# Kernel optimization log

Hardware: AMD Instinct MI355X
Metric: run time of the kernel (lower is better)

The kernel has to match this reference:

```python
import jax, jax.numpy as jnp
import numpy as np
import math

B, NQ, NS, K = 4, 4096, 16384, 16
P, IN, D = 3, 128, 256
H = D // 16   # nhead = out_dim // 16 = 16
HD = D // H   # head_dim = 16
RADIUS = 4.0
EPS = 1e-5


def _ln(x, g, b):
    m = jnp.mean(x, -1, keepdims=True)
    v = jnp.mean((x - m) ** 2, -1, keepdims=True)
    return (x - m) / jnp.sqrt(v + EPS) * g + b


def _pos_enc(x, W_pos, b_pos):
    # LearnablePositionalEncoding: cat([x, cos(Linear(2*pi*x))], -1)
    return jnp.concatenate([x, jnp.cos((2.0 * math.pi * x) @ W_pos + b_pos)], axis=-1)


def setup_inputs() -> dict:
    key = jax.random.key(0)
    ks = jax.random.split(key, 24)
    f32 = jnp.float32

    def w(k, shape):
        return jax.random.uniform(k, shape, f32, -1.0, 1.0) / np.float32(np.sqrt(shape[0]))

    inp = {}
    inp['q_pts'] = jax.random.normal(ks[0], (B, NQ, P), f32)
    inp['s_pts'] = jax.random.normal(ks[1], (B, NS, P), f32)
    inp['src_feats'] = jax.random.normal(ks[2], (B, NS, IN), f32)
    inp['query_feats'] = jax.random.normal(ks[3], (B, NQ, IN), f32)
    # shared proj (in_dim != out_dim, skip_dim=None -> skip_proj is the same Linear)
    inp['W_proj'] = w(ks[4], (IN, D)); inp['b_proj'] = jnp.zeros((D,), f32)
    # positional encoding Linear(p_dim, out_dim - p_dim)
    inp['W_pos'] = w(ks[5], (P, D - P)); inp['b_pos'] = jnp.zeros((D - P,), f32)
    # TransformerDecoderLayer (norm_first) params
    inp['ln1_g'] = jnp.ones((D,), f32); inp['ln1_b'] = jnp.zeros((D,), f32)
    inp['sa_Wv'] = w(ks[6], (D, D)); inp['sa_bv'] = jnp.zeros((D,), f32)
    inp['sa_Wo'] = w(ks[7], (D, D)); inp['sa_bo'] = jnp.zeros((D,), f32)
    inp['ln2_g'] = jnp.ones((D,), f32); inp['ln2_b'] = jnp.zeros((D,), f32)
    inp['ca_Wq'] = w(ks[8], (D, D)); inp['ca_bq'] = jnp.zeros((D,), f32)
    inp['ca_Wk'] = w(ks[9], (D, D)); inp['ca_bk'] = jnp.zeros((D,), f32)
    inp['ca_Wv'] = w(ks[10], (D, D)); inp['ca_bv'] = jnp.zeros((D,), f32)
    inp['ca_Wo'] = w(ks[11], (D, D)); inp['ca_bo'] = jnp.zeros((D,), f32)
    inp['ln3_g'] = jnp.ones((D,), f32); inp['ln3_b'] = jnp.zeros((D,), f32)
    inp['W1'] = w(ks[12], (D, D)); inp['b1'] = jnp.zeros((D,), f32)
    inp['W2'] = w(ks[13], (D, D)); inp['b2'] = jnp.zeros((D,), f32)
    inp['neighb_inds'] = jax.random.randint(ks[14], (B, NQ, K), 0, NS)
    return inp


def reference(q_pts, s_pts, src_feats, query_feats, W_proj, b_proj, W_pos, b_pos,
              ln1_g, ln1_b, sa_Wv, sa_bv, sa_Wo, sa_bo, ln2_g, ln2_b,
              ca_Wq, ca_bq, ca_Wk, ca_bk, ca_Wv, ca_bv, ca_Wo, ca_bo,
              ln3_g, ln3_b, W1, b1, W2, b2, neighb_inds):
    # append shadow point at 1e6 with zero feature row
    s_pts_ = jnp.concatenate([s_pts, jnp.full_like(s_pts[:, :1, :], 1e6)], axis=1)   # [B,NS+1,P]
    src_ = jnp.concatenate([src_feats, jnp.zeros_like(src_feats[:, :1, :])], axis=1)  # [B,NS+1,IN]
    src_p = src_ @ W_proj + b_proj            # proj(src_feats)  [B,NS+1,D]
    qf = query_feats @ W_proj + b_proj        # skip_proj == proj (skip_dim=None)
    inds = neighb_inds % (NS + 1)
    flat = inds.reshape(B, -1, 1)             # [B, NQ*K, 1]
    neighbors = jnp.take_along_axis(s_pts_, jnp.broadcast_to(flat, (B, NQ * K, P)), axis=1).reshape(B, NQ, K, P)
    neighb_x = jnp.take_along_axis(src_p, jnp.broadcast_to(flat, (B, NQ * K, D)), axis=1).reshape(B, NQ, K, D)
    neighbors = neighbors - q_pts[:, :, None, :]
    neighb_x = neighb_x + _pos_enc(neighbors / RADIUS, W_pos, b_pos)
    query_x = qf + _pos_enc(jnp.zeros_like(q_pts), W_pos, b_pos)
    mask = jnp.linalg.norm(neighbors, axis=-1) > RADIUS   # [B,NQ,K], True = invalid key

    x = query_x   # [B,NQ,D]: a length-1 target sequence per query point
    # --- self-attention block (seq len 1 -> softmax == 1 -> only V/O projections matter) ---
    h = _ln(x, ln1_g, ln1_b)
    x = x + (h @ sa_Wv + sa_bv) @ sa_Wo + sa_bo
    # --- cross-attention to K gathered neighbors ---
    h = _ln(x, ln2_g, ln2_b)
    q = (h @ ca_Wq + ca_bq).reshape(B, NQ, H, HD)
    kk = (neighb_x @ ca_Wk + ca_bk).reshape(B, NQ, K, H, HD)
    vv = (neighb_x @ ca_Wv + ca_bv).reshape(B, NQ, K, H, HD)
    scores = jnp.einsum('bnhd,bnkhd->bnhk', q, kk) / np.float32(np.sqrt(HD))
    scores = jnp.where(mask[:, :, None, :], jnp.float32(-1e9), scores)
    att = jax.nn.softmax(scores, axis=-1)
    ctx = jnp.einsum('bnhk,bnkhd->bnhd', att, vv).reshape(B, NQ, D)
    x = x + ctx @ ca_Wo + ca_bo
    # --- feed-forward (dim_feedforward == d_model, relu) ---
    h = _ln(x, ln3_g, ln3_b)
    x = x + jax.nn.relu(h @ W1 + b1) @ W2 + b2
    # original zeroes any NaNs (fully-masked rows); shapes chosen so this is a no-op
    return jnp.nan_to_num(x)
```

## Files before the change

### kernel.cpp

```cpp
#include <hip/hip_runtime.h>
#include <hip/hip_bf16.h>
#include <math.h>
#include <stdint.h>

typedef __attribute__((ext_vector_type(8))) short short8;
typedef __attribute__((ext_vector_type(4))) float floatx4;

#define DEVI __device__ __forceinline__

DEVI float b2f(unsigned short u) {
    union { unsigned int i; float f; } v; v.i = ((unsigned int)u) << 16; return v.f;
}
DEVI unsigned short f2b(float f) {
    unsigned int x = __float_as_uint(f);
    unsigned int r = (x + 0x7fffu + ((x >> 16) & 1u)) >> 16;
    return (unsigned short)r;
}

#define GLD16(gp, lp)                                                            \
    __builtin_amdgcn_global_load_lds(                                            \
        (__attribute__((address_space(1))) unsigned int*)(gp),                   \
        (__attribute__((address_space(3))) unsigned int*)(lp), 16, 0, 0)

static constexpr int NQ = 4096, NS = 16384;
static constexpr int NROW_Q = 4 * NQ;
static constexpr int NROW_S = 4 * NS;
static constexpr float INV2PI = 0.15915494309189535f;

__global__ void k_prep(const float* Wproj, const float* saWv, const float* saWo,
                       const float* caWq, const float* caWk, const float* caWv,
                       const float* caWo, const float* W1, const float* W2,
                       const float* b_pos,
                       unsigned short* wTproj, unsigned short* wTsaWv, unsigned short* wTsaWo,
                       unsigned short* wTcaWq, unsigned short* wTkv, unsigned short* wTcaWo,
                       unsigned short* wTW1, unsigned short* wTW2, float* penc0)
{
    int z = blockIdx.z;
    if (z == 9) {
        if (blockIdx.x == 0 && blockIdx.y == 0) {
            int c = threadIdx.y * 16 + threadIdx.x;
            float v = 0.f;
            if (c >= 3) {
                float rev = b_pos[c - 3] * INV2PI;
                rev -= floorf(rev);
                v = __builtin_amdgcn_cosf(rev);
            }
            penc0[c] = v;
        }
        return;
    }
    int n = blockIdx.x * 16 + threadIdx.x;
    int k = blockIdx.y * 16 + threadIdx.y;
    const float* src; unsigned short* dst; int K = 256;
    switch (z) {
        case 0: src = Wproj; dst = wTproj; K = 128; break;
        case 1: src = saWv;  dst = wTsaWv; break;
        case 2: src = saWo;  dst = wTsaWo; break;
        case 3: src = caWq;  dst = wTcaWq; break;
        case 4: src = caWk;  dst = wTkv;   break;
        case 5: src = caWv;  dst = wTkv + 256 * 256; break;
        case 6: src = caWo;  dst = wTcaWo; break;
        case 7: src = W1;    dst = wTW1;   break;
        default: src = W2;   dst = wTW2;   break;
    }
    if (k < K) dst[(size_t)n * K + k] = f2b(src[(size_t)k * 256 + n]);
}

__global__ void k_scale(const float* b_pos, float* bp2)
{
    int i = blockIdx.x * blockDim.x + threadIdx.x;
    if (i < 253) bp2[i] = b_pos[i] * INV2PI;
}

__global__ void k_cvt(const float* in, unsigned short* out, int n4)
{
    int i = blockIdx.x * blockDim.x + threadIdx.x;
    int stride = gridDim.x * blockDim.x;
    for (; i < n4; i += stride) {
        float4 v = ((const float4*)in)[i];
        unsigned long long p =
              (unsigned long long)f2b(v.x)
            | ((unsigned long long)f2b(v.y) << 16)
            | ((unsigned long long)f2b(v.z) << 32)
            | ((unsigned long long)f2b(v.w) << 48);
        ((unsigned long long*)out)[i] = p;
    }
}

template<int EPI>
__global__ __launch_bounds__(256, 2)
void k_gemm(const unsigned short* A, const unsigned short* BT, const float* bias,
            const float* extra, void* outp, int M, int N, int K)
{
    __shared__ alignas(16) unsigned short lA[128 * 64];
    __shared__ alignas(16) unsigned short lB[64 * 64];
    const int tid = threadIdx.x;
    const int wave = tid >> 6, lane = tid & 63;
    const int m0 = blockIdx.x * 128, n0 = blockIdx.y * 64;
    const int wm = (wave >> 1) * 64, wn = (wave & 1) * 32;
    floatx4 acc[4][2] = {};

    for (int kt = 0; kt < K; kt += 64) {
        __syncthreads();
        #pragma unroll
        for (int c = 0; c < 4; ++c) {
            int o = (tid + c * 256) * 16;
            int row = o >> 7, inner = o & 127;
            int srk = inner ^ ((row & 7) << 4);
            GLD16((const char*)A + ((size_t)(m0 + row) * K + kt) * 2 + srk, (char*)lA + o);
        }
        #pragma unroll
        for (int c = 0; c < 2; ++c) {
            int o = (tid + c * 256) * 16;
            int row = o >> 7, inner = o & 127;
            int srk = inner ^ ((row & 7) << 4);
            GLD16((const char*)BT + ((size_t)(n0 + row) * K + kt) * 2 + srk, (char*)lB + o);
        }
        __syncthreads();
        #pragma unroll
        for (int kc = 0; kc < 2; ++kc) {
            const int kb = kc * 64 + ((lane >> 4) << 4);
            short8 bf[2];
            #pragma unroll
            for (int nf = 0; nf < 2; ++nf) {
                int nn = wn + nf * 16 + (lane & 15);
                bf[nf] = *(const short8*)((const char*)lB + nn * 128 + (kb ^ ((nn & 7) << 4)));
            }
            #pragma unroll
            for (int mf = 0; mf < 4; ++mf) {
                int rr = wm + mf * 16 + (lane & 15);
                short8 af = *(const short8*)((const char*)lA + rr * 128 + (kb ^ ((rr & 7) << 4)));
                acc[mf][0] = __builtin_amdgcn_mfma_f32_16x16x32_bf16(af, bf[0], acc[mf][0], 0, 0, 0);
                acc[mf][1] = __builtin_amdgcn_mfma_f32_16x16x32_bf16(af, bf[1], acc[mf][1], 0, 0, 0);
            }
        }
    }
    #pragma unroll
    for (int mf = 0; mf < 4; ++mf)
        #pragma unroll
        for (int nf = 0; nf < 2; ++nf)
            #pragma unroll
            for (int r = 0; r < 4; ++r) {
                int row = m0 + wm + mf * 16 + ((lane >> 4) << 2) + r;
                int col = n0 + wn + nf * 16 + (lane & 15);
                float v = acc[mf][nf][r] + bias[col];
                if (EPI == 4) v += extra[(size_t)row * N + col];
                if (EPI == 1) v = fmaxf(v, 0.f);
                if (EPI == 4) {
                    if (isnan(v)) v = 0.f;
                    else if (isinf(v)) v = v > 0.f ? 3.402823466e38f : -3.402823466e38f;
                }
                if (EPI == 0 || EPI == 1)
                    ((unsigned short*)outp)[(size_t)row * N + col] = f2b(v);
                else
                    ((float*)outp)[(size_t)row * N + col] = v;
            }
}

template<int EPI2>
__global__ __launch_bounds__(256, 2)
void k_gemm_ln(const unsigned short* A, const unsigned short* BT, const float* bias,
               const float* extra, const float* lng, const float* lnb,
               float* outf, unsigned short* outb, int M, int K)
{
    __shared__ alignas(16) unsigned short lA[64 * 64];
    __shared__ alignas(16) unsigned short lB[256 * 64];
    const int tid = threadIdx.x, wave = tid >> 6, lane = tid & 63;
    const int l15 = lane & 15, lg = lane >> 4;
    const int m0 = blockIdx.x * 64;
    floatx4 acc[16] = {};

    for (int kt = 0; kt < K; kt += 64) {
        __syncthreads();
        #pragma unroll
        for (int c = 0; c < 2; ++c) {
            int o = (tid + c * 256) * 16;
            int row = o >> 7, inner = o & 127;
            int srk = inner ^ ((row & 7) << 4);
            GLD16((const char*)A + ((size_t)(m0 + row) * K + kt) * 2 + srk, (char*)lA + o);
        }
        #pragma unroll
        for (int c = 0; c < 8; ++c) {
            int o = (tid + c * 256) * 16;
            int row = o >> 7, inner = o & 127;
            int srk = inner ^ ((row & 7) << 4);
            GLD16((const char*)BT + ((size_t)row * K + kt) * 2 + srk, (char*)lB + o);
        }
        __syncthreads();
        #pragma unroll
        for (int kc = 0; kc < 2; ++kc) {
            const int kb = kc * 64 + (lg << 4);
            int rr = wave * 16 + l15;
            short8 af = *(const short8*)((const char*)lA + rr * 128 + (kb ^ ((rr & 7) << 4)));
            #pragma unroll
            for (int nf = 0; nf < 16; ++nf) {
                int nn = nf * 16 + l15;
                short8 bf = *(const short8*)((const char*)lB + nn * 128 + (kb ^ ((nn & 7) << 4)));
                acc[nf] = __builtin_amdgcn_mfma_f32_16x16x32_bf16(af, bf, acc[nf], 0, 0, 0);
            }
        }
    }

    #pragma unroll
    for (int nf = 0; nf < 16; ++nf) {
        int col = nf * 16 + l15;
        float bi = bias[col] + (EPI2 == 0 ? extra[col] : 0.f);
        #pragma unroll
        for (int r = 0; r < 4; ++r) {
            int row = m0 + wave * 16 + lg * 4 + r;
            float v = acc[nf][r] + bi;
            if (EPI2 == 1) v += extra[(size_t)row * 256 + col];
            acc[nf][r] = v;
            outf[(size_t)row * 256 + col] = v;
        }
    }
    float mean[4], inv[4];
    #pragma unroll
    for (int r = 0; r < 4; ++r) {
        float s = 0.f;
        #pragma unroll
        for (int nf = 0; nf < 16; ++nf) s += acc[nf][r];
        #pragma unroll
        for (int t = 1; t <= 8; t <<= 1) s += __shfl_xor(s, t);
        mean[r] = s * (1.f / 256.f);
        float q = 0.f;
        #pragma unroll
        for (int nf = 0; nf < 16; ++nf) { float d = acc[nf][r] - mean[r]; q += d * d; }
        #pragma unroll
        for (int t = 1; t <= 8; t <<= 1) q += __shfl_xor(q, t);
        inv[r] = 1.0f / sqrtf(q * (1.f / 256.f) + 1e-5f);
    }
    #pragma unroll
    for (int nf = 0; nf < 16; ++nf) {
        int col = nf * 16 + l15;
        float g = lng[col], b = lnb[col];
        #pragma unroll
        for (int r = 0; r < 4; ++r) {
            int row = m0 + wave * 16 + lg * 4 + r;
            outb[(size_t)row * 256 + col] = f2b((acc[nf][r] - mean[r]) * inv[r] * g + b);
        }
    }
}

__global__ __launch_bounds__(256, 3)
void k_attn(const unsigned short* srcp, const unsigned short* qb, const int* inds,
            const float* s_pts, const float* q_pts, const float* W_pos, const float* bp2,
            const unsigned short* wTkv, const float* bv, unsigned short* ctx)
{
    __shared__ alignas(16) unsigned short nx[64 * 256];
    __shared__ alignas(16) float att_lds[4 * 16 * 16];
    __shared__ alignas(16) float dist_lds[64];
    const int tid = threadIdx.x, wave = tid >> 6, lane = tid & 63;
    const int qbase = blockIdx.x * 4;
    const int l15 = lane & 15, lg = lane >> 4;

    float qv[4][4], bvv[4];
    #pragma unroll
    for (int mf = 0; mf < 4; ++mf)
        #pragma unroll
        for (int nf = 0; nf < 4; ++nf)
            qv[mf][nf] = b2f(qb[(size_t)(qbase + mf) * 256 + (wave * 4 + nf) * 16 + l15]) * 0.25f;
    #pragma unroll
    for (int nf = 0; nf < 4; ++nf) bvv[nf] = bv[(wave * 4 + nf) * 16 + l15];

    {
        int r = tid >> 2, sub = tid & 3;
        int qi = qbase + (r >> 4);
        int bb = qi >> 12;
        int k = r & 15;
        int raw = inds[((size_t)qi << 4) + k];
        int idx = raw % (NS + 1); if (idx < 0) idx += NS + 1;
        bool shadow = (idx == NS);
        const int c0 = sub * 64;
        const unsigned short* srow = srcp + ((size_t)bb * NS + (shadow ? 0 : idx)) * 256 + c0;
        short8 sv[8];
        #pragma unroll
        for (int j = 0; j < 8; ++j) sv[j] = *(const short8*)(srow + j * 8);

        float px = q_pts[(size_t)qi * 3], py = q_pts[(size_t)qi * 3 + 1], pz = q_pts[(size_t)qi * 3 + 2];
        float sx, sy, sz;
        if (shadow) { sx = sy = sz = 1e6f; }
        else {
            const float* sp = s_pts + ((size_t)bb * NS + idx) * 3;
            sx = sp[0]; sy = sp[1]; sz = sp[2];
        }
        float tx = (sx - px) * 0.25f, ty = (sy - py) * 0.25f, tz = (sz - pz) * 0.25f;
        if (sub == 0) dist_lds[r] = tx * tx + ty * ty + tz * tz;

        #pragma unroll
        for (int cc = 0; cc < 64; cc += 8) {
            short8 vals;
            #pragma unroll
            for (int j = 0; j < 8; ++j) {
                int c = c0 + cc + j;
                float pe;
                if (c == 0) pe = tx;
                else if (c == 1) pe = ty;
                else if (c == 2) pe = tz;
                else {
                    int jj = c - 3;
                    float rev = fmaf(tx, W_pos[jj],
                                fmaf(ty, W_pos[253 + jj],
                                fmaf(tz, W_pos[506 + jj], bp2[jj])));
                    rev -= floorf(rev);
                    pe = __builtin_amdgcn_cosf(rev);
                }
                float sval = shadow ? 0.f : b2f((unsigned short)sv[cc / 8][j]);
                vals[j] = (short)f2b(sval + pe);
            }
            int byte = (c0 + cc) * 2;
            *(short8*)((char*)nx + r * 512 + (byte ^ ((r & 7) << 4))) = vals;
        }
    }
    __syncthreads();

    const int wn = wave * 64;
    floatx4 acc[4][4];

    #pragma unroll
    for (int mf = 0; mf < 4; ++mf)
        #pragma unroll
        for (int nf = 0; nf < 4; ++nf) acc[mf][nf] = floatx4{0.f, 0.f, 0.f, 0.f};

    #pragma unroll 2
    for (int kt = 0; kt < 8; ++kt) {
        const int kb = kt * 64 + (lg << 4);
        short8 bfr[4];
        #pragma unroll
        for (int nf = 0; nf < 4; ++nf) {
            int nn = wn + nf * 16 + l15;
            bfr[nf] = *(const short8*)((const char*)wTkv + (size_t)nn * 512 + kt * 64 + (lg << 4));
        }
        #pragma unroll
        for (int mf = 0; mf < 4; ++mf) {
            int rr = mf * 16 + l15;
            short8 af = *(const short8*)((const char*)nx + rr * 512 + (kb ^ ((rr & 7) << 4)));
            #pragma unroll
            for (int nf = 0; nf < 4; ++nf)
                acc[mf][nf] = __builtin_amdgcn_mfma_f32_16x16x32_bf16(af, bfr[nf], acc[mf][nf], 0, 0, 0);
        }
    }

    {
        #pragma unroll
        for (int mf = 0; mf < 4; ++mf) {
            float4 d4 = *(const float4*)&dist_lds[mf * 16 + lg * 4];
            float dd4[4] = {d4.x, d4.y, d4.z, d4.w};
            #pragma unroll
            for (int nf = 0; nf < 4; ++nf) {
                float s[4];
                #pragma unroll
                for (int rr = 0; rr < 4; ++rr) s[rr] = acc[mf][nf][rr] * qv[mf][nf];
                #pragma unroll
                for (int t = 1; t <= 8; t <<= 1)
                    #pragma unroll
                    for (int rr = 0; rr < 4; ++rr) s[rr] += __shfl_xor(s[rr], t);
                #pragma unroll
                for (int rr = 0; rr < 4; ++rr)
                    s[rr] = (dd4[rr] > 1.0f) ? -1e9f : s[rr];
                float m = fmaxf(fmaxf(s[0], s[1]), fmaxf(s[2], s[3]));
                m = fmaxf(m, __shfl_xor(m, 16));
                m = fmaxf(m, __shfl_xor(m, 32));
                float p[4], su = 0.f;
                #pragma unroll
                for (int rr = 0; rr < 4; ++rr) { p[rr] = __expf(s[rr] - m); su += p[rr]; }
                su += __shfl_xor(su, 16);
                su += __shfl_xor(su, 32);
                float inv = __builtin_amdgcn_rcpf(su);
                if (l15 == 0) {
                    float4 a4 = {p[0] * inv, p[1] * inv, p[2] * inv, p[3] * inv};
                    *(float4*)&att_lds[(mf * 16 + wave * 4 + nf) * 16 + lg * 4] = a4;
                }
            }
        }
    }

    #pragma unroll
    for (int mf = 0; mf < 4; ++mf)
        #pragma unroll
        for (int nf = 0; nf < 4; ++nf) acc[mf][nf] = floatx4{0.f, 0.f, 0.f, 0.f};

    #pragma unroll 2
    for (int kt = 0; kt < 8; ++kt) {
        const int kb = kt * 64 + (lg << 4);
        short8 bfr[4];
        #pragma unroll
        for (int nf = 0; nf < 4; ++nf) {
            int nn = 256 + wn + nf * 16 + l15;
            bfr[nf] = *(const short8*)((const char*)wTkv + (size_t)nn * 512 + kt * 64 + (lg << 4));
        }
        #pragma unroll
        for (int mf = 0; mf < 4; ++mf) {
            int rr = mf * 16 + l15;
            short8 af = *(const short8*)((const char*)nx + rr * 512 + (kb ^ ((rr & 7) << 4)));
            #pragma unroll
            for (int nf = 0; nf < 4; ++nf)
                acc[mf][nf] = __builtin_amdgcn_mfma_f32_16x16x32_bf16(af, bfr[nf], acc[mf][nf], 0, 0, 0);
        }
    }

    {
        #pragma unroll
        for (int mf = 0; mf < 4; ++mf)
            #pragma unroll
            for (int nf = 0; nf < 4; ++nf) {
                float4 a4 = *(const float4*)&att_lds[(mf * 16 + wave * 4 + nf) * 16 + lg * 4];
                float o = a4.x * acc[mf][nf][0];
                o = fmaf(a4.y, acc[mf][nf][1], o);
                o = fmaf(a4.z, acc[mf][nf][2], o);
                o = fmaf(a4.w, acc[mf][nf][3], o);
                o += __shfl_xor(o, 16);
                o += __shfl_xor(o, 32);
                o += bvv[nf];
                if (lane < 16)
                    ctx[(size_t)(qbase + mf) * 256 + (wave * 4 + nf) * 16 + lane] = f2b(o);
            }
    }
}

extern "C" void kernel_launch(void* const* d_in, const int* in_sizes, int n_in,
                              void* d_out, int out_size, void* d_ws, size_t ws_size,
                              hipStream_t stream)
{
    const float* q_pts   = (const float*)d_in[0];
    const float* s_pts   = (const float*)d_in[1];
    const float* src_f   = (const float*)d_in[2];
    const float* query_f = (const float*)d_in[3];
    const float* W_proj  = (const float*)d_in[4];
    const float* b_proj  = (const float*)d_in[5];
    const float* W_pos   = (const float*)d_in[6];
    const float* b_pos   = (const float*)d_in[7];
    const float* ln1_g   = (const float*)d_in[8];
    const float* ln1_b   = (const float*)d_in[9];
    const float* sa_Wv   = (const float*)d_in[10];
    const float* sa_bv   = (const float*)d_in[11];
    const float* sa_Wo   = (const float*)d_in[12];
    const float* sa_bo   = (const float*)d_in[13];
    const float* ln2_g   = (const float*)d_in[14];
    const float* ln2_b   = (const float*)d_in[15];
    const float* ca_Wq   = (const float*)d_in[16];
    const float* ca_bq   = (const float*)d_in[17];
    const float* ca_Wk   = (const float*)d_in[18];
    const float* ca_Wv   = (const float*)d_in[20];
    const float* ca_bv   = (const float*)d_in[21];
    const float* ca_Wo   = (const float*)d_in[22];
    const float* ca_bo   = (const float*)d_in[23];
    const float* ln3_g   = (const float*)d_in[24];
    const float* ln3_b   = (const float*)d_in[25];
    const float* W1      = (const float*)d_in[26];
    const float* b1      = (const float*)d_in[27];
    const float* W2      = (const float*)d_in[28];
    const float* b2      = (const float*)d_in[29];
    const int*   inds    = (const int*)d_in[30];

    char* ws = (char*)d_ws;
    size_t off = 0;
    auto alloc = [&](size_t bytes) { char* p = ws + off; off += (bytes + 1023) & ~(size_t)1023; return p; };

    unsigned short* wTproj = (unsigned short*)alloc(256 * 128 * 2);
    unsigned short* wTsaWv = (unsigned short*)alloc(256 * 256 * 2);
    unsigned short* wTsaWo = (unsigned short*)alloc(256 * 256 * 2);
    unsigned short* wTcaWq = (unsigned short*)alloc(256 * 256 * 2);
    unsigned short* wTkv   = (unsigned short*)alloc(512 * 256 * 2);
    unsigned short* wTcaWo = (unsigned short*)alloc(256 * 256 * 2);
    unsigned short* wTW1   = (unsigned short*)alloc(256 * 256 * 2);
    unsigned short* wTW2   = (unsigned short*)alloc(256 * 256 * 2);
    float*          penc0  = (float*)alloc(256 * 4);
    float*          bp2    = (float*)alloc(256 * 4);
    unsigned short* srcb   = (unsigned short*)alloc((size_t)NROW_S * 128 * 2);
    unsigned short* qfb    = (unsigned short*)alloc((size_t)NROW_Q * 128 * 2);
    unsigned short* srcp   = (unsigned short*)alloc((size_t)NROW_S * 256 * 2);
    float*          qx     = (float*)alloc((size_t)NROW_Q * 256 * 4);
    unsigned short* hbuf   = (unsigned short*)alloc((size_t)NROW_Q * 256 * 2);
    unsigned short* tbuf   = (unsigned short*)alloc((size_t)NROW_Q * 256 * 2);
    float*          xbuf   = (float*)alloc((size_t)NROW_Q * 256 * 4);
    unsigned short* qbuf   = (unsigned short*)alloc((size_t)NROW_Q * 256 * 2);
    unsigned short* ctxbuf = (unsigned short*)alloc((size_t)NROW_Q * 256 * 2);
    float*          x2buf  = (float*)alloc((size_t)NROW_Q * 256 * 4);

    dim3 bl16(16, 16);
    k_prep<<<dim3(16, 16, 10), bl16, 0, stream>>>(
        W_proj, sa_Wv, sa_Wo, ca_Wq, ca_Wk, ca_Wv, ca_Wo, W1, W2, b_pos,
        wTproj, wTsaWv, wTsaWo, wTcaWq, wTkv, wTcaWo, wTW1, wTW2, penc0);
    k_scale<<<1, 256, 0, stream>>>(b_pos, bp2);

    k_cvt<<<1024, 256, 0, stream>>>(src_f, srcb, NROW_S * 128 / 4);
    k_cvt<<<1024, 256, 0, stream>>>(query_f, qfb, NROW_Q * 128 / 4);

    k_gemm<0><<<dim3(512, 4), 256, 0, stream>>>(srcb, wTproj, b_proj, nullptr, srcp, NROW_S, 256, 128);
    k_gemm_ln<0><<<256, 256, 0, stream>>>(qfb, wTproj, b_proj, penc0, ln1_g, ln1_b,
                                          qx, hbuf, NROW_Q, 128);

    k_gemm<0><<<dim3(128, 4), 256, 0, stream>>>(hbuf, wTsaWv, sa_bv, nullptr, tbuf, NROW_Q, 256, 256);
    k_gemm_ln<1><<<256, 256, 0, stream>>>(tbuf, wTsaWo, sa_bo, qx, ln2_g, ln2_b,
                                          xbuf, hbuf, NROW_Q, 256);

    k_gemm<0><<<dim3(128, 4), 256, 0, stream>>>(hbuf, wTcaWq, ca_bq, nullptr, qbuf, NROW_Q, 256, 256);
    k_attn<<<4096, 256, 0, stream>>>(srcp, qbuf, inds, s_pts, q_pts, W_pos, bp2, wTkv, ca_bv, ctxbuf);
    k_gemm_ln<1><<<256, 256, 0, stream>>>(ctxbuf, wTcaWo, ca_bo, xbuf, ln3_g, ln3_b,
                                          x2buf, hbuf, NROW_Q, 256);

    k_gemm<1><<<dim3(128, 4), 256, 0, stream>>>(hbuf, wTW1, b1, nullptr, tbuf, NROW_Q, 256, 256);
    k_gemm<4><<<dim3(128, 4), 256, 0, stream>>>(tbuf, wTW2, b2, x2buf, d_out, NROW_Q, 256, 256);

    (void)in_sizes; (void)n_in; (void)out_size; (void)ws_size;
}
```

Baseline: 394.2 us.

## Transpose MFMA operands in attention kernel so softmax reduces with DPP

Swaps the MFMA A/B operands so each accumulator holds head-dim values along rows and neighbors along lanes. The softmax over 16 neighbors then becomes a within-row DPP reduction instead of xor shuffles. Attention weights stay in registers rather than round-tripping through LDS. The query values are staged in LDS, and the output is written as packed bf16 pairs. The aim is to cut shuffle and LDS traffic in the attention epilogue. In exchange it adds LDS reads of the query, and correctness depends on the DPP row patterns and the transposed layout being right.

Measured after the change: 402.2 us. +2.0%, slower.

```diff
diff --git a/kernel.cpp b/kernel.cpp
--- a/kernel.cpp
+++ b/kernel.cpp
@@ -21,6 +21,12 @@
     __builtin_amdgcn_global_load_lds(                                            \
         (__attribute__((address_space(1))) unsigned int*)(gp),                   \
         (__attribute__((address_space(3))) unsigned int*)(lp), 16, 0, 0)
+
+#define DPPF(x, ctrl) __int_as_float(__builtin_amdgcn_mov_dpp(__float_as_int(x), ctrl, 0xf, 0xf, true))
+#define DPP_MAX16(x) do { x = fmaxf(x, DPPF(x, 0xB1)); x = fmaxf(x, DPPF(x, 0x4E)); \
+                          x = fmaxf(x, DPPF(x, 0x141)); x = fmaxf(x, DPPF(x, 0x140)); } while (0)
+#define DPP_SUM16(x) do { x += DPPF(x, 0xB1); x += DPPF(x, 0x4E); \
+                          x += DPPF(x, 0x141); x += DPPF(x, 0x140); } while (0)
 
 static constexpr int NQ = 4096, NS = 16384;
 static constexpr int NROW_Q = 4 * NQ;
@@ -248,20 +254,22 @@
             const unsigned short* wTkv, const float* bv, unsigned short* ctx)
 {
     __shared__ alignas(16) unsigned short nx[64 * 256];
-    __shared__ alignas(16) float att_lds[4 * 16 * 16];
+    __shared__ alignas(16) float qls[4 * 256];
     __shared__ alignas(16) float dist_lds[64];
     const int tid = threadIdx.x, wave = tid >> 6, lane = tid & 63;
     const int qbase = blockIdx.x * 4;
     const int l15 = lane & 15, lg = lane >> 4;
 
-    float qv[4][4], bvv[4];
-    #pragma unroll
-    for (int mf = 0; mf < 4; ++mf)
-        #pragma unroll
-        for (int nf = 0; nf < 4; ++nf)
-            qv[mf][nf] = b2f(qb[(size_t)(qbase + mf) * 256 + (wave * 4 + nf) * 16 + l15]) * 0.25f;
-    #pragma unroll
-    for (int nf = 0; nf < 4; ++nf) bvv[nf] = bv[(wave * 4 + nf) * 16 + l15];
+    {
+        int q = tid >> 6, c4 = (tid & 63) * 4;
+        unsigned long long qp = *(const unsigned long long*)(qb + (size_t)(qbase + q) * 256 + c4);
+        float4 qf;
+        qf.x = b2f((unsigned short)(qp)) * 0.25f;
+        qf.y = b2f((unsigned short)(qp >> 16)) * 0.25f;
+        qf.z = b2f((unsigned short)(qp >> 32)) * 0.25f;
+        qf.w = b2f((unsigned short)(qp >> 48)) * 0.25f;
+        *(float4*)&qls[q * 256 + c4] = qf;
+    }
 
     {
         int r = tid >> 2, sub = tid & 3;
@@ -318,9 +326,9 @@
     floatx4 acc[4][4];
 
     #pragma unroll
-    for (int mf = 0; mf < 4; ++mf)
-        #pragma unroll
-        for (int nf = 0; nf < 4; ++nf) acc[mf][nf] = floatx4{0.f, 0.f, 0.f, 0.f};
+    for (int nf = 0; nf < 4; ++nf)
+        #pragma unroll
+        for (int mf = 0; mf < 4; ++mf) acc[nf][mf] = floatx4{0.f, 0.f, 0.f, 0.f};
 
     #pragma unroll 2
     for (int kt = 0; kt < 8; ++kt) {
@@ -337,48 +345,35 @@
             short8 af = *(const short8*)((const char*)nx + rr * 512 + (kb ^ ((rr & 7) << 4)));
             #pragma unroll
             for (int nf = 0; nf < 4; ++nf)
-                acc[mf][nf] = __builtin_amdgcn_mfma_f32_16x16x32_bf16(af, bfr[nf], acc[mf][nf], 0, 0, 0);
-        }
-    }
-
-    {
-        #pragma unroll
-        for (int mf = 0; mf < 4; ++mf) {
-            float4 d4 = *(const float4*)&dist_lds[mf * 16 + lg * 4];
-            float dd4[4] = {d4.x, d4.y, d4.z, d4.w};
-            #pragma unroll
-            for (int nf = 0; nf < 4; ++nf) {
-                float s[4];
-                #pragma unroll
-                for (int rr = 0; rr < 4; ++rr) s[rr] = acc[mf][nf][rr] * qv[mf][nf];
-                #pragma unroll
-                for (int t = 1; t <= 8; t <<= 1)
-                    #pragma unroll
-                    for (int rr = 0; rr < 4; ++rr) s[rr] += __shfl_xor(s[rr], t);
-                #pragma unroll
-                for (int rr = 0; rr < 4; ++rr)
-                    s[rr] = (dd4[rr] > 1.0f) ? -1e9f : s[rr];
-                float m = fmaxf(fmaxf(s[0], s[1]), fmaxf(s[2], s[3]));
-                m = fmaxf(m, __shfl_xor(m, 16));
-                m = fmaxf(m, __shfl_xor(m, 32));
-                float p[4], su = 0.f;
-                #pragma unroll
-                for (int rr = 0; rr < 4; ++rr) { p[rr] = __expf(s[rr] - m); su += p[rr]; }
-                su += __shfl_xor(su, 16);
-                su += __shfl_xor(su, 32);
-                float inv = __builtin_amdgcn_rcpf(su);
-                if (l15 == 0) {
-                    float4 a4 = {p[0] * inv, p[1] * inv, p[2] * inv, p[3] * inv};
-                    *(float4*)&att_lds[(mf * 16 + wave * 4 + nf) * 16 + lg * 4] = a4;
-                }
-            }
-        }
-    }
-
-    #pragma unroll
-    for (int mf = 0; mf < 4; ++mf)
-        #pragma unroll
-        for (int nf = 0; nf < 4; ++nf) acc[mf][nf] = floatx4{0.f, 0.f, 0.f, 0.f};
+                acc[nf][mf] = __builtin_amdgcn_mfma_f32_16x16x32_bf16(bfr[nf], af, acc[nf][mf], 0, 0, 0);
+        }
+    }
+
+    float p[4][4];
+    #pragma unroll
+    for (int mf = 0; mf < 4; ++mf) {
+        float dmask = dist_lds[mf * 16 + l15];
+        #pragma unroll
+        for (int nf = 0; nf < 4; ++nf) {
+            float4 q4 = *(const float4*)&qls[mf * 256 + (wave * 4 + nf) * 16 + lg * 4];
+            float s = acc[nf][mf][0] * q4.x;
+            s = fmaf(acc[nf][mf][1], q4.y, s);
+            s = fmaf(acc[nf][mf][2], q4.z, s);
+            s = fmaf(acc[nf][mf][3], q4.w, s);
+            s += __shfl_xor(s, 16);
+            s += __shfl_xor(s, 32);
+            s = (dmask > 1.0f) ? -1e9f : s;
+            float m = s; DPP_MAX16(m);
+            float e = __expf(s - m);
+            float su = e; DPP_SUM16(su);
+            p[nf][mf] = e * __builtin_amdgcn_rcpf(su);
+        }
+    }
+
+    #pragma unroll
+    for (int nf = 0; nf < 4; ++nf)
+        #pragma unroll
+        for (int mf = 0; mf < 4; ++mf) acc[nf][mf] = floatx4{0.f, 0.f, 0.f, 0.f};
 
     #pragma unroll 2
     for (int kt = 0; kt < 8; ++kt) {
@@ -395,27 +390,28 @@
             short8 af = *(const short8*)((const char*)nx + rr * 512 + (kb ^ ((rr & 7) << 4)));
             #pragma unroll
             for (int nf = 0; nf < 4; ++nf)
-                acc[mf][nf] = __builtin_amdgcn_mfma_f32_16x16x32_bf16(af, bfr[nf], acc[mf][nf], 0, 0, 0);
-        }
-    }
-
-    {
-        #pragma unroll
-        for (int mf = 0; mf < 4; ++mf)
-            #pragma unroll
-            for (int nf = 0; nf < 4; ++nf) {
-                float4 a4 = *(const float4*)&att_lds[(mf * 16 + wave * 4 + nf) * 16 + lg * 4];
-                float o = a4.x * acc[mf][nf][0];
-                o = fmaf(a4.y, acc[mf][nf][1], o);
-                o = fmaf(a4.z, acc[mf][nf][2], o);
-                o = fmaf(a4.w, acc[mf][nf][3], o);
-                o += __shfl_xor(o, 16);
-                o += __shfl_xor(o, 32);
-                o += bvv[nf];
-                if (lane < 16)
-                    ctx[(size_t)(qbase + mf) * 256 + (wave * 4 + nf) * 16 + lane] = f2b(o);
-            }
-    }
+                acc[nf][mf] = __builtin_amdgcn_mfma_f32_16x16x32_bf16(bfr[nf], af, acc[nf][mf], 0, 0, 0);
+        }
+    }
+
+    #pragma unroll
+    for (int mf = 0; mf < 4; ++mf)
+        #pragma unroll
+        for (int nf = 0; nf < 4; ++nf) {
+            float o0 = p[nf][mf] * acc[nf][mf][0];
+            float o1 = p[nf][mf] * acc[nf][mf][1];
+            float o2 = p[nf][mf] * acc[nf][mf][2];
+            float o3 = p[nf][mf] * acc[nf][mf][3];
+            DPP_SUM16(o0); DPP_SUM16(o1); DPP_SUM16(o2); DPP_SUM16(o3);
+            if (l15 == 0) {
+                int h16 = (wave * 4 + nf) * 16 + lg * 4;
+                const float4 bq = *(const float4*)(bv + h16);
+                unsigned int w0, w1;
+                asm("v_cvt_pk_bf16_f32 %0, %1, %2" : "=v"(w0) : "v"(o0 + bq.x), "v"(o1 + bq.y));
+                asm("v_cvt_pk_bf16_f32 %0, %1, %2" : "=v"(w1) : "v"(o2 + bq.z), "v"(o3 + bq.w));
+                *(uint2*)(ctx + (size_t)(qbase + mf) * 256 + h16) = make_uint2(w0, w1);
+            }
+        }
 }
 
 extern "C" void kernel_launch(void* const* d_in, const int* in_sizes, int n_in,
```
